# Kernel optimization log

Measured on AMD Instinct MI355X. Metric: run time of the kernel, lower is better.

The kernel has to match this reference:

```python
import jax, jax.numpy as jnp
import numpy as np


def setup_inputs() -> dict:
    key = jax.random.key(0)
    k1, k2, k3, k4 = jax.random.split(key, 4)
    b, c, h, w = 4, 256, 64, 64
    Fq_l = jax.random.normal(k1, (b, c, h, w), dtype=jnp.float32)
    Fp_l = jax.random.normal(k2, (b, c, h, w), dtype=jnp.float32)
    # 1x1 conv: weight [out=c//2, in=c], bias [c//2]
    W = jax.random.normal(k3, (c // 2, c), dtype=jnp.float32) * (1.0 / np.sqrt(c))
    bias = jax.random.normal(k4, (c // 2,), dtype=jnp.float32) * 0.01
    return {"Fq_l": Fq_l, "Fp_l": Fp_l, "W": W, "bias": bias}


def reference(Fq_l, Fp_l, W, bias):
    b, c, h, w = Fq_l.shape
    hw = h * w
    # 1x1 conv == per-pixel linear projection
    q = jnp.einsum('oc,bchw->bohw', W, Fq_l) + bias[None, :, None, None]
    p = jnp.einsum('oc,bchw->bohw', W, Fp_l) + bias[None, :, None, None]
    qf = q.reshape(b, -1, hw)  # [b, c/2, hw]
    pf = p.reshape(b, -1, hw)
    qf = qf / jnp.linalg.norm(qf, axis=1, keepdims=True)
    pf = pf / jnp.linalg.norm(pf, axis=1, keepdims=True)
    # cosine similarity, [b, hw, hw]
    sim = jnp.einsum('bcn,bcm->bnm', qf, pf)
    idx = jnp.argmax(sim, axis=-1)  # [b, hw]
    Fp_flat = Fp_l.reshape(b, c, hw)
    aligned = jnp.take_along_axis(Fp_flat, idx[:, None, :], axis=2)  # [b, c, hw]
    return aligned.reshape(b, c, h, w)
```

## Files before the change

kernel.cpp:

```cpp
#include <hip/hip_runtime.h>

#define HW 4096
#define LCAP 1536

typedef short bf16x8 __attribute__((ext_vector_type(8)));
typedef float f32x16 __attribute__((ext_vector_type(16)));

__device__ __forceinline__ ushort f2bf_rne(float f) {
    unsigned u = __float_as_uint(f);
    return (ushort)((u + 0x7FFFu + ((u >> 16) & 1u)) >> 16);
}

__global__ __launch_bounds__(256) void init_kernel(
    unsigned long long* __restrict__ best)
{
    int i = blockIdx.x * 256 + threadIdx.x;
    best[i] = 0ull;
}

__global__ __launch_bounds__(256) void transpose_w_kernel(
    const float* __restrict__ Wm, float* __restrict__ Wt)
{
    const int o = blockIdx.x;
    const int c = threadIdx.x;
    Wt[c * 128 + o] = Wm[o * 256 + c];
}

__global__ __launch_bounds__(256) void proj_kernel(
    const float* __restrict__ Fq, const float* __restrict__ Fp,
    const float* __restrict__ Wt, const float* __restrict__ bias,
    float* __restrict__ Qt, float* __restrict__ Pt,
    ushort* __restrict__ Qpk, ushort* __restrict__ Ppk,
    float* __restrict__ qnorm)
{
    __shared__ float Ws[64][128];
    __shared__ float Xs[64][64];
    __shared__ float psum[16][68];

    const int tid = threadIdx.x;
    const int z  = blockIdx.z;
    const float* __restrict__ X = z ? Fp : Fq;
    const int b  = blockIdx.y;
    const int n0 = blockIdx.x * 64;
    const int og = tid >> 4;
    const int ng = tid & 15;

    float acc[4][8];
    #pragma unroll
    for (int i = 0; i < 4; ++i)
        #pragma unroll
        for (int j = 0; j < 8; ++j) acc[i][j] = 0.f;

    for (int cc = 0; cc < 4; ++cc) {
        __syncthreads();
        {
            const float4* src = (const float4*)(Wt + (size_t)cc * 64 * 128);
            float4* dst = (float4*)Ws;
            #pragma unroll
            for (int it = 0; it < 8; ++it) dst[it * 256 + tid] = src[it * 256 + tid];
        }
        #pragma unroll
        for (int it = 0; it < 4; ++it) {
            int f = it * 256 + tid;
            int r = f >> 4, n4 = f & 15;
            *(float4*)&Xs[r][n4 * 4] =
                *(const float4*)&X[(size_t)(b * 256 + cc * 64 + r) * HW + n0 + n4 * 4];
        }
        __syncthreads();

        for (int r = 0; r < 64; ++r) {
            float4 w0 = *(const float4*)&Ws[r][og * 8];
            float4 w1 = *(const float4*)&Ws[r][og * 8 + 4];
            float4 xv = *(const float4*)&Xs[r][ng * 4];
            float wa[8] = {w0.x, w0.y, w0.z, w0.w, w1.x, w1.y, w1.z, w1.w};
            float xa[4] = {xv.x, xv.y, xv.z, xv.w};
            #pragma unroll
            for (int i = 0; i < 4; ++i)
                #pragma unroll
                for (int j = 0; j < 8; ++j)
                    acc[i][j] += wa[j] * xa[i];
        }
    }

    {
        float4 b0 = *(const float4*)&bias[og * 8];
        float4 b1 = *(const float4*)&bias[og * 8 + 4];
        float ba[8] = {b0.x, b0.y, b0.z, b0.w, b1.x, b1.y, b1.z, b1.w};
        #pragma unroll
        for (int i = 0; i < 4; ++i)
            #pragma unroll
            for (int j = 0; j < 8; ++j) acc[i][j] += ba[j];
    }

    #pragma unroll
    for (int i = 0; i < 4; ++i) {
        float s = 0.f;
        #pragma unroll
        for (int j = 0; j < 8; ++j) s += acc[i][j] * acc[i][j];
        psum[og][ng * 4 + i] = s;
    }
    __syncthreads();
    float tot[4];
    #pragma unroll
    for (int i = 0; i < 4; ++i) {
        float s = 0.f;
        #pragma unroll
        for (int g = 0; g < 16; ++g) s += psum[g][ng * 4 + i];
        tot[i] = s;
    }

    if (z) {
        #pragma unroll
        for (int i = 0; i < 4; ++i) {
            float s = 1.0f / sqrtf(tot[i]);
            #pragma unroll
            for (int j = 0; j < 8; ++j) acc[i][j] *= s;
        }
    } else if (og == 0) {
        #pragma unroll
        for (int i = 0; i < 4; ++i)
            qnorm[b * HW + n0 + ng * 4 + i] = sqrtf(tot[i]);
    }

    {
        float* __restrict__ T = z ? Pt : Qt;
        #pragma unroll
        for (int i = 0; i < 4; ++i) {
            size_t tb = ((size_t)b * HW + n0 + ng * 4 + i) * 128 + og * 8;
            *(float4*)&T[tb]     = make_float4(acc[i][0], acc[i][1], acc[i][2], acc[i][3]);
            *(float4*)&T[tb + 4] = make_float4(acc[i][4], acc[i][5], acc[i][6], acc[i][7]);
        }
    }
    {
        ushort* __restrict__ PK = z ? Ppk : Qpk;
        const int ks = og >> 1;
        #pragma unroll
        for (int i = 0; i < 4; ++i) {
            const int na  = n0 + ng * 4 + i;
            const int t32 = na >> 5;
            const int lt  = (na & 31) + 32 * (og & 1);
            ushort u[8];
            #pragma unroll
            for (int k = 0; k < 8; ++k) u[k] = f2bf_rne(acc[i][k]);
            size_t pk = ((((size_t)b * 128 + t32) * 8 + ks) * 64 + lt) * 8;
            uint4 w;
            w.x = (unsigned)u[0] | ((unsigned)u[1] << 16);
            w.y = (unsigned)u[2] | ((unsigned)u[3] << 16);
            w.z = (unsigned)u[4] | ((unsigned)u[5] << 16);
            w.w = (unsigned)u[6] | ((unsigned)u[7] << 16);
            *(uint4*)&PK[pk] = w;
        }
    }
}

__global__ __launch_bounds__(256, 2) void sim_sketch_kernel(
    const ushort* __restrict__ Qpk, const ushort* __restrict__ Ppk,
    const float* __restrict__ qnorm,
    float* __restrict__ Vmax, unsigned char* __restrict__ SK)
{
    __shared__ ushort Qs[16384];
    __shared__ ushort Bs[16384];

    const int tid  = threadIdx.x;
    const int lane = tid & 63;
    const int w    = tid >> 6;
    const int nb   = blockIdx.x;
    const int b    = blockIdx.y;
    const int ms   = blockIdx.z;
    const int hi   = lane >> 5;

    {
        const uint4* src = (const uint4*)(Qpk + ((size_t)b * 128 + nb * 4) * 4096);
        uint4* dst = (uint4*)Qs;
        #pragma unroll
        for (int it = 0; it < 8; ++it) dst[it * 256 + tid] = src[it * 256 + tid];
    }

    float rq[16];
    #pragma unroll
    for (int r = 0; r < 16; ++r) {
        int nl_ = (r & 3) + 8 * (r >> 2) + 4 * hi;
        rq[r] = 256.0f / qnorm[b * HW + nb * 128 + w * 32 + nl_];
    }

    const size_t g16f = (size_t)b * 256 + (size_t)(nb * 4 + w) * 2 + hi;
    const int mb0 = ms * 1024 + (lane & 31);

    float bestv[16];
    #pragma unroll
    for (int r = 0; r < 16; ++r) bestv[r] = -1e30f;

    for (int ch = 0; ch < 8; ++ch) {
        __syncthreads();
        {
            const uint4* src = (const uint4*)(Ppk +
                ((size_t)b * 128 + ms * 32 + ch * 4) * 4096);
            uint4* dst = (uint4*)Bs;
            #pragma unroll
            for (int it = 0; it < 8; ++it) dst[it * 256 + tid] = src[it * 256 + tid];
        }
        __syncthreads();

        for (int mtl = 0; mtl < 4; ++mtl) {
            f32x16 acc;
            #pragma unroll
            for (int r = 0; r < 16; ++r) acc[r] = 0.f;
            #pragma unroll
            for (int ks = 0; ks < 8; ++ks) {
                bf16x8 a  = *(const bf16x8*)&Qs[((w   * 8 + ks) * 64 + lane) * 8];
                bf16x8 bb = *(const bf16x8*)&Bs[((mtl * 8 + ks) * 64 + lane) * 8];
                acc = __builtin_amdgcn_mfma_f32_32x32x16_bf16(a, bb, acc, 0, 0, 0);
            }
            #pragma unroll
            for (int r = 0; r < 16; ++r)
                bestv[r] = fmaxf(bestv[r], acc[r]);

            unsigned dw[4] = {0u, 0u, 0u, 0u};
            #pragma unroll
            for (int r = 0; r < 16; ++r) {
                float x = acc[r] * rq[r];
#if __has_builtin(__builtin_amdgcn_cvt_pk_u8_f32)
                dw[r >> 2] = (unsigned)__builtin_amdgcn_cvt_pk_u8_f32(
                    x, (unsigned)(r & 3), (int)dw[r >> 2]);
#else
                int vi = (int)rintf(x);
                vi = vi < 0 ? 0 : (vi > 255 ? 255 : vi);
                dw[r >> 2] |= (unsigned)vi << (8 * (r & 3));
#endif
            }
            const int m = mb0 + ch * 128 + mtl * 32;
            uint4 pk;
            pk.x = dw[0]; pk.y = dw[1]; pk.z = dw[2]; pk.w = dw[3];
            *(uint4*)(SK + ((g16f * 4096 + (size_t)m) << 4)) = pk;
        }
    }

    #pragma unroll
    for (int r = 0; r < 16; ++r) {
        float v = bestv[r];
        #pragma unroll
        for (int d = 1; d < 32; d <<= 1)
            v = fmaxf(v, __shfl_xor(v, d, 64));
        if ((lane & 31) == 0) {
            int nl_ = (r & 3) + 8 * (r >> 2) + 4 * hi;
            int na = nb * 128 + w * 32 + nl_;
            Vmax[((size_t)b * HW + na) * 4 + ms] = v;
        }
    }
}

__global__ __launch_bounds__(256) void thresh_kernel(
    const float* __restrict__ Vmax, const float* __restrict__ qnorm,
    unsigned char* __restrict__ t8pk)
{
    int i = blockIdx.x * 256 + threadIdx.x;
    float g = -1e30f;
    #pragma unroll
    for (int s = 0; s < 4; ++s) g = fmaxf(g, Vmax[(size_t)i * 4 + s]);
    float qn  = qnorm[i];
    float thr = g - (0.016f * qn + 1e-6f);
    float scl = 256.0f / qn;
    int t = (int)floorf(thr * scl) - 1;
    t = t < 0 ? 0 : (t > 255 ? 255 : t);
    int b = i >> 12, n = i & 4095;
    int nl = n & 31;
    int j   = (nl & 3) + 4 * (nl >> 3);
    int g16 = (n >> 5) * 2 + ((nl >> 2) & 1);
    t8pk[(((size_t)b * 256 + g16) << 4) + j] = (unsigned char)t;
}

__device__ __noinline__ void dot_one_slow(
    const float* Qsrow, const float* __restrict__ Pt,
    int b, int m, int n, unsigned long long* __restrict__ best)
{
    const float4* __restrict__ pr = (const float4*)&Pt[((size_t)b * HW + m) * 128];
    float acc = 0.f;
    #pragma unroll
    for (int k = 0; k < 32; ++k) {
        float4 pv = pr[k];
        float4 qv = *(const float4*)&Qsrow[k * 4];
        acc += qv.x * pv.x + qv.y * pv.y + qv.z * pv.z + qv.w * pv.w;
    }
    unsigned u = __float_as_uint(acc);
    unsigned kk = (u & 0x80000000u) ? ~u : (u | 0x80000000u);
    unsigned long long key = ((unsigned long long)kk << 32) | (unsigned)(4095 - m);
    atomicMax(&best[(size_t)b * HW + n], key);
}

__global__ __launch_bounds__(256) void scan_rescore_kernel(
    const unsigned char* __restrict__ SK, const unsigned char* __restrict__ t8pk,
    const float* __restrict__ Qt, const float* __restrict__ Pt,
    unsigned long long* __restrict__ best)
{
    __shared__ float Qs[16][132];
    __shared__ int nlist[16];
    __shared__ ushort hl[LCAP];
    __shared__ unsigned lcnt;

    const int fg  = blockIdx.x;
    const int tid = threadIdx.x;
    const int b = fg >> 8, g = fg & 255, t = g >> 1, gs = g & 1;

    if (tid == 0) lcnt = 0u;
    if (tid < 16) {
        nlist[tid] = t * 32 + (tid & 3) + 8 * (tid >> 2) + 4 * gs;
    }
    __syncthreads();

    #pragma unroll
    for (int it = 0; it < 2; ++it) {
        int idx = it * 256 + tid;
        int row = idx >> 5, c4 = (idx & 31) * 4;
        *(float4*)&Qs[row][c4] =
            *(const float4*)&Qt[((size_t)b * HW + nlist[row]) * 128 + c4];
    }

    int myt[16];
    {
        uint4 tv = *(const uint4*)&t8pk[(size_t)fg << 4];
        unsigned ta[4] = {tv.x, tv.y, tv.z, tv.w};
        #pragma unroll
        for (int d = 0; d < 4; ++d)
            #pragma unroll
            for (int k = 0; k < 4; ++k)
                myt[d * 4 + k] = (int)((ta[d] >> (8 * k)) & 255u);
    }
    __syncthreads();

    const unsigned char* __restrict__ row = SK + ((size_t)fg << 16);
    for (int it = 0; it < 16; ++it) {
        const int m = it * 256 + tid;
        uint4 v = *(const uint4*)(row + ((size_t)m << 4));
        unsigned wv[4] = {v.x, v.y, v.z, v.w};
        #pragma unroll
        for (int d = 0; d < 4; ++d) {
            #pragma unroll
            for (int k = 0; k < 4; ++k) {
                int bv = (int)((wv[d] >> (8 * k)) & 255u);
                if (bv >= myt[d * 4 + k]) {
                    const int j = d * 4 + k;
                    unsigned pos = atomicAdd(&lcnt, 1u);
                    if (pos < LCAP) {
                        hl[pos] = (ushort)((j << 12) | m);
                    } else {
                        dot_one_slow(&Qs[j][0], Pt, b, m, nlist[j], best);
                    }
                }
            }
        }
    }

    __syncthreads();
    unsigned cnt = lcnt < LCAP ? lcnt : LCAP;
    for (unsigned p = tid; p < cnt; p += 256) {
        int e = hl[p];
        int j = e >> 12, m = e & 4095;
        const float4* __restrict__ pr = (const float4*)&Pt[((size_t)b * HW + m) * 128];
        float acc = 0.f;
        #pragma unroll
        for (int k = 0; k < 32; ++k) {
            float4 pv = pr[k];
            float4 qv = *(const float4*)&Qs[j][k * 4];
            acc += qv.x * pv.x + qv.y * pv.y + qv.z * pv.z + qv.w * pv.w;
        }
        unsigned u = __float_as_uint(acc);
        unsigned kk = (u & 0x80000000u) ? ~u : (u | 0x80000000u);
        unsigned long long key = ((unsigned long long)kk << 32) | (unsigned)(4095 - m);
        atomicMax(&best[(size_t)b * HW + nlist[j]], key);
    }
}

__global__ __launch_bounds__(256) void gather_kernel(
    const float* __restrict__ Fp, const unsigned long long* __restrict__ best,
    float* __restrict__ out)
{
    __shared__ float row[4096];
    const int blk = blockIdx.x;
    const int c = blk & 255;
    const int b = blk >> 8;
    const int tid = threadIdx.x;

    const float* __restrict__ src = Fp + ((size_t)b * 256 + c) * HW;
    #pragma unroll
    for (int it = 0; it < 4; ++it) {
        int f = it * 256 + tid;
        *(float4*)&row[f * 4] = *(const float4*)&src[f * 4];
    }
    __syncthreads();

    float* __restrict__ dst = out + ((size_t)b * 256 + c) * HW;
    #pragma unroll
    for (int it = 0; it < 16; ++it) {
        int n = it * 256 + tid;
        int m = 4095 - (int)(best[(size_t)b * HW + n] & 0xFFFull);
        dst[n] = row[m];
    }
}

extern "C" void kernel_launch(void* const* d_in, const int* in_sizes, int n_in,
                              void* d_out, int out_size, void* d_ws, size_t ws_size,
                              hipStream_t stream) {
    const float* Fq   = (const float*)d_in[0];
    const float* Fp   = (const float*)d_in[1];
    const float* Wm   = (const float*)d_in[2];
    const float* bias = (const float*)d_in[3];
    float* out = (float*)d_out;

    char* base = (char*)d_ws;
    float*  Qt    = (float*)(base);
    float*  Pt    = (float*)(base + (8u << 20));
    ushort* Qpk   = (ushort*)(base + (16u << 20));
    ushort* Ppk   = (ushort*)(base + (20u << 20));
    unsigned char* SK = (unsigned char*)(base + (24u << 20));
    char* x = base + (88u << 20);
    float*  qnorm = (float*)x;              x += 65536;
    float*  Vmax  = (float*)x;              x += 262144;
    unsigned char* t8pk = (unsigned char*)x; x += 16384;
    unsigned long long* best = (unsigned long long*)x; x += 131072;
    float*  Wtg   = (float*)x;

    init_kernel<<<64, 256, 0, stream>>>(best);
    transpose_w_kernel<<<128, 256, 0, stream>>>(Wm, Wtg);
    proj_kernel<<<dim3(64, 4, 2), 256, 0, stream>>>(Fq, Fp, Wtg, bias,
                                                    Qt, Pt, Qpk, Ppk, qnorm);
    sim_sketch_kernel<<<dim3(32, 4, 4), 256, 0, stream>>>(Qpk, Ppk, qnorm,
                                                          Vmax, SK);
    thresh_kernel<<<64, 256, 0, stream>>>(Vmax, qnorm, t8pk);
    scan_rescore_kernel<<<1024, 256, 0, stream>>>(SK, t8pk, Qt, Pt, best);
    gather_kernel<<<1024, 256, 0, stream>>>(Fp, best, out);
}
```

Measured before the change: 167.6 us.

## Add per-column max sketch to skip SK reads, fold init/thresh into scan

The sim kernel now keeps Q fragments in registers and streams P fragments straight from global memory, dropping the LDS staging and block barriers. It also emits a one-byte per-column maximum (CM), so the scan kernel reads the full 16-byte sketch only when that maximum reaches the group's lowest threshold. The init and thresh kernels are removed; their work moves into the scan kernel prologue. This cuts launches and most of the sketch read traffic, at the cost of extra byte stores in the sim kernel and global-load latency on the MFMA path.

```diff
diff --git a/kernel.cpp b/kernel.cpp
--- a/kernel.cpp
+++ b/kernel.cpp
@@ -9,13 +9,6 @@
 __device__ __forceinline__ ushort f2bf_rne(float f) {
     unsigned u = __float_as_uint(f);
     return (ushort)((u + 0x7FFFu + ((u >> 16) & 1u)) >> 16);
-}
-
-__global__ __launch_bounds__(256) void init_kernel(
-    unsigned long long* __restrict__ best)
-{
-    int i = blockIdx.x * 256 + threadIdx.x;
-    best[i] = 0ull;
 }
 
 __global__ __launch_bounds__(256) void transpose_w_kernel(
@@ -156,11 +149,9 @@
 __global__ __launch_bounds__(256, 2) void sim_sketch_kernel(
     const ushort* __restrict__ Qpk, const ushort* __restrict__ Ppk,
     const float* __restrict__ qnorm,
-    float* __restrict__ Vmax, unsigned char* __restrict__ SK)
-{
-    __shared__ ushort Qs[16384];
-    __shared__ ushort Bs[16384];
-
+    float* __restrict__ Vmax, unsigned char* __restrict__ SK,
+    unsigned char* __restrict__ CM)
+{
     const int tid  = threadIdx.x;
     const int lane = tid & 63;
     const int w    = tid >> 6;
@@ -169,12 +160,12 @@
     const int ms   = blockIdx.z;
     const int hi   = lane >> 5;
 
-    {
-        const uint4* src = (const uint4*)(Qpk + ((size_t)b * 128 + nb * 4) * 4096);
-        uint4* dst = (uint4*)Qs;
-        #pragma unroll
-        for (int it = 0; it < 8; ++it) dst[it * 256 + tid] = src[it * 256 + tid];
-    }
+    const ushort* __restrict__ qbase =
+        Qpk + ((size_t)(b * 128 + nb * 4)) * 4096 + (size_t)lane * 8;
+    bf16x8 qf[8];
+    #pragma unroll
+    for (int ks = 0; ks < 8; ++ks)
+        qf[ks] = *(const bf16x8*)(qbase + (w * 8 + ks) * 512);
 
     float rq[16];
     #pragma unroll
@@ -190,40 +181,43 @@
     #pragma unroll
     for (int r = 0; r < 16; ++r) bestv[r] = -1e30f;
 
+    #pragma unroll 1
     for (int ch = 0; ch < 8; ++ch) {
-        __syncthreads();
-        {
-            const uint4* src = (const uint4*)(Ppk +
-                ((size_t)b * 128 + ms * 32 + ch * 4) * 4096);
-            uint4* dst = (uint4*)Bs;
-            #pragma unroll
-            for (int it = 0; it < 8; ++it) dst[it * 256 + tid] = src[it * 256 + tid];
-        }
-        __syncthreads();
-
+        const ushort* __restrict__ pbase =
+            Ppk + ((size_t)(b * 128 + ms * 32 + ch * 4)) * 4096 + (size_t)lane * 8;
+        #pragma unroll 2
         for (int mtl = 0; mtl < 4; ++mtl) {
             f32x16 acc;
             #pragma unroll
             for (int r = 0; r < 16; ++r) acc[r] = 0.f;
             #pragma unroll
             for (int ks = 0; ks < 8; ++ks) {
-                bf16x8 a  = *(const bf16x8*)&Qs[((w   * 8 + ks) * 64 + lane) * 8];
-                bf16x8 bb = *(const bf16x8*)&Bs[((mtl * 8 + ks) * 64 + lane) * 8];
-                acc = __builtin_amdgcn_mfma_f32_32x32x16_bf16(a, bb, acc, 0, 0, 0);
+                bf16x8 bb = *(const bf16x8*)(pbase + (mtl * 8 + ks) * 512);
+                acc = __builtin_amdgcn_mfma_f32_32x32x16_bf16(qf[ks], bb, acc, 0, 0, 0);
             }
             #pragma unroll
             for (int r = 0; r < 16; ++r)
                 bestv[r] = fmaxf(bestv[r], acc[r]);
 
+            float x[16];
+            #pragma unroll
+            for (int r = 0; r < 16; ++r) x[r] = acc[r] * rq[r];
+
+            float c0 = fmaxf(fmaxf(fmaxf(x[0], x[1]), fmaxf(x[2], x[3])),
+                             fmaxf(fmaxf(x[4], x[5]), fmaxf(x[6], x[7])));
+            float c1 = fmaxf(fmaxf(fmaxf(x[8], x[9]), fmaxf(x[10], x[11])),
+                             fmaxf(fmaxf(x[12], x[13]), fmaxf(x[14], x[15])));
+            int cmi = (int)(fmaxf(c0, c1) + 0.5f) + 1;
+            cmi = cmi < 0 ? 0 : (cmi > 255 ? 255 : cmi);
+
             unsigned dw[4] = {0u, 0u, 0u, 0u};
             #pragma unroll
             for (int r = 0; r < 16; ++r) {
-                float x = acc[r] * rq[r];
 #if __has_builtin(__builtin_amdgcn_cvt_pk_u8_f32)
                 dw[r >> 2] = (unsigned)__builtin_amdgcn_cvt_pk_u8_f32(
-                    x, (unsigned)(r & 3), (int)dw[r >> 2]);
+                    x[r], (unsigned)(r & 3), (int)dw[r >> 2]);
 #else
-                int vi = (int)rintf(x);
+                int vi = (int)rintf(x[r]);
                 vi = vi < 0 ? 0 : (vi > 255 ? 255 : vi);
                 dw[r >> 2] |= (unsigned)vi << (8 * (r & 3));
 #endif
@@ -232,6 +226,7 @@
             uint4 pk;
             pk.x = dw[0]; pk.y = dw[1]; pk.z = dw[2]; pk.w = dw[3];
             *(uint4*)(SK + ((g16f * 4096 + (size_t)m) << 4)) = pk;
+            CM[g16f * 4096 + (size_t)m] = (unsigned char)cmi;
         }
     }
 
@@ -249,26 +244,6 @@
     }
 }
 
-__global__ __launch_bounds__(256) void thresh_kernel(
-    const float* __restrict__ Vmax, const float* __restrict__ qnorm,
-    unsigned char* __restrict__ t8pk)
-{
-    int i = blockIdx.x * 256 + threadIdx.x;
-    float g = -1e30f;
-    #pragma unroll
-    for (int s = 0; s < 4; ++s) g = fmaxf(g, Vmax[(size_t)i * 4 + s]);
-    float qn  = qnorm[i];
-    float thr = g - (0.016f * qn + 1e-6f);
-    float scl = 256.0f / qn;
-    int t = (int)floorf(thr * scl) - 1;
-    t = t < 0 ? 0 : (t > 255 ? 255 : t);
-    int b = i >> 12, n = i & 4095;
-    int nl = n & 31;
-    int j   = (nl & 3) + 4 * (nl >> 3);
-    int g16 = (n >> 5) * 2 + ((nl >> 2) & 1);
-    t8pk[(((size_t)b * 256 + g16) << 4) + j] = (unsigned char)t;
-}
-
 __device__ __noinline__ void dot_one_slow(
     const float* Qsrow, const float* __restrict__ Pt,
     int b, int m, int n, unsigned long long* __restrict__ best)
@@ -288,12 +263,14 @@
 }
 
 __global__ __launch_bounds__(256) void scan_rescore_kernel(
-    const unsigned char* __restrict__ SK, const unsigned char* __restrict__ t8pk,
+    const unsigned char* __restrict__ SK, const unsigned char* __restrict__ CM,
+    const float* __restrict__ Vmax, const float* __restrict__ qnorm,
     const float* __restrict__ Qt, const float* __restrict__ Pt,
     unsigned long long* __restrict__ best)
 {
     __shared__ float Qs[16][132];
     __shared__ int nlist[16];
+    __shared__ int t8s[16];
     __shared__ ushort hl[LCAP];
     __shared__ unsigned lcnt;
 
@@ -303,7 +280,17 @@
 
     if (tid == 0) lcnt = 0u;
     if (tid < 16) {
-        nlist[tid] = t * 32 + (tid & 3) + 8 * (tid >> 2) + 4 * gs;
+        int n = t * 32 + (tid & 3) + 8 * (tid >> 2) + 4 * gs;
+        nlist[tid] = n;
+        best[(size_t)b * HW + n] = 0ull;
+        float gmax = -1e30f;
+        #pragma unroll
+        for (int s = 0; s < 4; ++s)
+            gmax = fmaxf(gmax, Vmax[((size_t)b * HW + n) * 4 + s]);
+        float qn  = qnorm[b * HW + n];
+        float thr = gmax - (0.016f * qn + 1e-6f);
+        int tt = (int)floorf(thr * (256.0f / qn)) - 1;
+        t8s[tid] = tt < 0 ? 0 : (tt > 255 ? 255 : tt);
     }
     __syncthreads();
 
@@ -316,34 +303,41 @@
     }
 
     int myt[16];
-    {
-        uint4 tv = *(const uint4*)&t8pk[(size_t)fg << 4];
-        unsigned ta[4] = {tv.x, tv.y, tv.z, tv.w};
-        #pragma unroll
-        for (int d = 0; d < 4; ++d)
-            #pragma unroll
-            for (int k = 0; k < 4; ++k)
-                myt[d * 4 + k] = (int)((ta[d] >> (8 * k)) & 255u);
-    }
+    #pragma unroll
+    for (int j = 0; j < 16; ++j) myt[j] = t8s[j];
+    int gmin = myt[0];
+    #pragma unroll
+    for (int j = 1; j < 16; ++j) gmin = min(gmin, myt[j]);
     __syncthreads();
 
-    const unsigned char* __restrict__ row = SK + ((size_t)fg << 16);
-    for (int it = 0; it < 16; ++it) {
-        const int m = it * 256 + tid;
-        uint4 v = *(const uint4*)(row + ((size_t)m << 4));
-        unsigned wv[4] = {v.x, v.y, v.z, v.w};
-        #pragma unroll
-        for (int d = 0; d < 4; ++d) {
-            #pragma unroll
-            for (int k = 0; k < 4; ++k) {
-                int bv = (int)((wv[d] >> (8 * k)) & 255u);
-                if (bv >= myt[d * 4 + k]) {
-                    const int j = d * 4 + k;
-                    unsigned pos = atomicAdd(&lcnt, 1u);
-                    if (pos < LCAP) {
-                        hl[pos] = (ushort)((j << 12) | m);
-                    } else {
-                        dot_one_slow(&Qs[j][0], Pt, b, m, nlist[j], best);
+    const unsigned char* __restrict__ cmrow = CM + ((size_t)fg << 12);
+    const unsigned char* __restrict__ skrow = SK + ((size_t)fg << 16);
+
+    #pragma unroll
+    for (int it = 0; it < 4; ++it) {
+        int m0 = (it * 256 + tid) * 4;
+        unsigned cm4 = *(const unsigned*)(cmrow + m0);
+        #pragma unroll
+        for (int k = 0; k < 4; ++k) {
+            int cmv = (int)((cm4 >> (8 * k)) & 255u);
+            if (cmv >= gmin) {
+                int m = m0 + k;
+                uint4 v = *(const uint4*)(skrow + ((size_t)m << 4));
+                unsigned wv[4] = {v.x, v.y, v.z, v.w};
+                #pragma unroll
+                for (int d = 0; d < 4; ++d) {
+                    #pragma unroll
+                    for (int kk = 0; kk < 4; ++kk) {
+                        int bv = (int)((wv[d] >> (8 * kk)) & 255u);
+                        int j = d * 4 + kk;
+                        if (bv >= myt[j]) {
+                            unsigned pos = atomicAdd(&lcnt, 1u);
+                            if (pos < LCAP) {
+                                hl[pos] = (ushort)((j << 12) | m);
+                            } else {
+                                dot_one_slow(&Qs[j][0], Pt, b, m, nlist[j], best);
+                            }
+                        }
                     }
                 }
             }
@@ -412,20 +406,19 @@
     ushort* Qpk   = (ushort*)(base + (16u << 20));
     ushort* Ppk   = (ushort*)(base + (20u << 20));
     unsigned char* SK = (unsigned char*)(base + (24u << 20));
-    char* x = base + (88u << 20);
+    unsigned char* CM = (unsigned char*)(base + (88u << 20));
+    char* x = base + (92u << 20);
     float*  qnorm = (float*)x;              x += 65536;
     float*  Vmax  = (float*)x;              x += 262144;
-    unsigned char* t8pk = (unsigned char*)x; x += 16384;
     unsigned long long* best = (unsigned long long*)x; x += 131072;
     float*  Wtg   = (float*)x;
 
-    init_kernel<<<64, 256, 0, stream>>>(best);
     transpose_w_kernel<<<128, 256, 0, stream>>>(Wm, Wtg);
     proj_kernel<<<dim3(64, 4, 2), 256, 0, stream>>>(Fq, Fp, Wtg, bias,
                                                     Qt, Pt, Qpk, Ppk, qnorm);
     sim_sketch_kernel<<<dim3(32, 4, 4), 256, 0, stream>>>(Qpk, Ppk, qnorm,
-                                                          Vmax, SK);
-    thresh_kernel<<<64, 256, 0, stream>>>(Vmax, qnorm, t8pk);
-    scan_rescore_kernel<<<1024, 256, 0, stream>>>(SK, t8pk, Qt, Pt, best);
+                                                          Vmax, SK, CM);
+    scan_rescore_kernel<<<1024, 256, 0, stream>>>(SK, CM, Vmax, qnorm,
+                                                  Qt, Pt, best);
     gather_kernel<<<1024, 256, 0, stream>>>(Fp, best, out);
 }
```

Measured after the change: 184.7 us. 1.1x slower.
